# Optimization experiments

Hardware: AMD Instinct MI355X
Metric: run time of the kernel (lower is better)

## Reference

```python
import jax, jax.numpy as jnp
import numpy as np

B_SZ, SEQ = 16, 2048
VOCAB, EMBED = 50257, 128
DSTATE, HID, NCLS = 16, 256, 10
NEDGE = 8192  # edges per graph (avg degree 4)
LN_EPS = 1e-5


def setup_inputs() -> dict:
    key = jax.random.key(0)
    ks = jax.random.split(key, 12)
    tokens = jax.random.randint(ks[0], (B_SZ, SEQ), 0, VOCAB, dtype=jnp.int32)
    lengths = jnp.full((B_SZ,), SEQ, dtype=jnp.int32)  # full-length graphs
    edge_indices = jax.random.randint(ks[1], (B_SZ, 2, NEDGE), 0, SEQ, dtype=jnp.int32)
    emb = (jax.random.normal(ks[2], (VOCAB, EMBED)) * 0.02).at[0].set(0.0)  # padding_idx=0
    A_log = jax.random.normal(ks[3], (EMBED, DSTATE)) * 0.1
    B_w = jax.random.normal(ks[4], (DSTATE, EMBED)) * (1.0 / np.sqrt(EMBED))
    C_w = jax.random.normal(ks[5], (EMBED, DSTATE)) * (1.0 / np.sqrt(DSTATE))
    D_skip = jnp.ones((EMBED,))
    ln_g = jnp.ones((EMBED,))
    ln_b = jnp.zeros((EMBED,))
    Wmsg_w = jax.random.normal(ks[6], (HID, EMBED)) * (1.0 / np.sqrt(EMBED))
    Wupd_w = jax.random.normal(ks[7], (HID, EMBED + HID)) * (1.0 / np.sqrt(EMBED + HID))
    Wupd_b = jax.random.normal(ks[8], (HID,)) * 0.01
    cls_w = jax.random.normal(ks[9], (NCLS, HID)) * (1.0 / np.sqrt(HID))
    cls_b = jnp.zeros((NCLS,))
    return {"tokens": tokens, "lengths": lengths, "edge_indices": edge_indices,
            "emb": emb, "A_log": A_log, "B_w": B_w, "C_w": C_w, "D_skip": D_skip,
            "ln_g": ln_g, "ln_b": ln_b, "Wmsg_w": Wmsg_w, "Wupd_w": Wupd_w,
            "Wupd_b": Wupd_b, "cls_w": cls_w, "cls_b": cls_b}


def _ssm(x, A_log, B_w, C_w, D_skip, ln_g, ln_b):
    # x: (B, S, d_model). Diagonal SSM: h_t = h_{t-1}*exp(A) + B x_t (broadcast over d_model)
    Aexp = jnp.exp(-jnp.exp(A_log))  # (d_model, d_state)
    h0 = jnp.zeros((x.shape[0], EMBED, DSTATE), dtype=x.dtype)

    def step(h, x_t):  # x_t: (B, d_model)
        b_t = x_t @ B_w.T                            # (B, d_state)
        h = h * Aexp[None] + b_t[:, None, :]          # (B, d_model, d_state)
        y = h.mean(axis=1) @ C_w.T + D_skip * x_t     # (B, d_model)
        return h, y

    _, ys = jax.lax.scan(step, h0, jnp.swapaxes(x, 0, 1))
    out = jnp.swapaxes(ys, 0, 1)                      # (B, S, d_model)
    mu = out.mean(-1, keepdims=True)
    var = jnp.mean((out - mu) ** 2, axis=-1, keepdims=True)
    return ln_g * (out - mu) * jax.lax.rsqrt(var + LN_EPS) + ln_b


def reference(tokens, lengths, edge_indices, emb, A_log, B_w, C_w, D_skip,
              ln_g, ln_b, Wmsg_w, Wupd_w, Wupd_b, cls_w, cls_b):
    x = emb[tokens]                                   # (B, S, E)
    h = _ssm(x, A_log, B_w, C_w, D_skip, ln_g, ln_b)  # (B, S, E)
    src, dst = edge_indices[:, 0, :], edge_indices[:, 1, :]   # (B, Ne)
    h_src = jnp.take_along_axis(h, src[:, :, None], axis=1)   # (B, Ne, E)
    msgs = jnp.einsum('bed,hd->beh', h_src, Wmsg_w)            # (B, Ne, H)
    flat_dst = (jnp.arange(B_SZ, dtype=dst.dtype)[:, None] * SEQ + dst).reshape(-1)
    agg = jax.ops.segment_sum(msgs.reshape(-1, HID), flat_dst,
                              num_segments=B_SZ * SEQ).reshape(B_SZ, SEQ, HID)
    upd = jax.nn.relu(jnp.concatenate([h, agg], axis=-1) @ Wupd_w.T + Wupd_b)  # (B, S, H)
    pooled = upd.mean(axis=1)                          # (B, H)  (all lengths == SEQ)
    return pooled @ cls_w.T + cls_b                    # (B, NCLS)
```

## Files before the change

### kernel.cpp

```cpp
#include <hip/hip_runtime.h>

#define B_SZ   16
#define SEQ    2048
#define VOCAB  50257
#define EMBED  128
#define DSTATE 16
#define HID    256
#define NCLS   10
#define NEDGE  8192
#define KTR    64
#define LN_EPS 1e-5f
#define NROW   (B_SZ*SEQ)
#define BCAP   32
#define OVCAP  1024

#define PB_CAST   4096
#define PB_BUCKET (PB_CAST + 512)
#define PB_PRECM  (PB_BUCKET + 128)
#define PB_CTAB   (PB_PRECM + 16)
#define PB_TOTAL  (PB_CTAB + 1)

typedef float  f32x4 __attribute__((ext_vector_type(4)));
typedef short  s16x8 __attribute__((ext_vector_type(8)));

__device__ __forceinline__ float scrub(float x){
  return (x == x && fabsf(x) < 1e30f) ? x : 0.f;
}
__device__ __forceinline__ short f2b(float f){
  unsigned int u = __float_as_uint(f);
  unsigned int r = (u + 0x7fffu + ((u >> 16) & 1u)) >> 16;
  return (short)r;
}
__device__ __forceinline__ unsigned int pack2(float a, float b){
  return (unsigned int)(unsigned short)f2b(a)
       | ((unsigned int)(unsigned short)f2b(b) << 16);
}
__device__ __forceinline__ float lo2f(unsigned int v){ return __uint_as_float(v << 16); }
__device__ __forceinline__ float hi2f(unsigned int v){ return __uint_as_float(v & 0xffff0000u); }

__global__ __launch_bounds__(256) void k_prep(
    const int* __restrict__ tokens, const float* __restrict__ emb,
    const float* __restrict__ A_log, const float* __restrict__ B_w,
    const float* __restrict__ Wmsg, const float* __restrict__ Wupd,
    const int* __restrict__ edges,
    float* __restrict__ c_tab, short* __restrict__ Bf, float* __restrict__ MT,
    unsigned int* __restrict__ x_bf, int* __restrict__ cnt,
    unsigned short* __restrict__ bucket, int* __restrict__ ovf_cnt,
    int* __restrict__ ovf){
  int bid = blockIdx.x, tid = threadIdx.x;
  if (bid < PB_CAST){
    int gid = bid*256 + tid;
    int row = gid >> 5, ch = gid & 31;
    int tok = tokens[row];
    tok = tok < 0 ? 0 : (tok >= VOCAB ? VOCAB-1 : tok);
    float4 v = *(const float4*)(emb + (size_t)tok*EMBED + ch*4);
    uint2 o; o.x = pack2(v.x, v.y); o.y = pack2(v.z, v.w);
    *(uint2*)(x_bf + (size_t)row*(EMBED/2) + ch*2) = o;
  } else if (bid < PB_BUCKET){
    int eid = (bid-PB_CAST)*256 + tid;
    int b = eid >> 13, i = eid & (NEDGE-1);
    const int* ei = edges + (size_t)b*2*NEDGE;
    int s = ei[i]         & (SEQ-1);
    int d = ei[NEDGE + i] & (SEQ-1);
    int gdst = (b << 11) | d;
    int slot = atomicAdd(&cnt[gdst], 1);
    if (slot < BCAP) bucket[(size_t)gdst*BCAP + slot] = (unsigned short)s;
    else {
      int o = atomicAdd(ovf_cnt, 1);
      if (o < OVCAP) ovf[o] = ((b << 11) | s) | (gdst << 16);
    }
  } else if (bid < PB_PRECM){
    int hp = (bid-PB_BUCKET)*2 + (tid >> 7);
    int e  = tid & 127;
    const float* w2 = Wupd + (size_t)hp*384 + 128;
    float acc = 0.f;
    for (int h1 = 0; h1 < HID; ++h1)
      acc += Wmsg[h1*EMBED + e] * w2[h1];
    MT[(size_t)hp*EMBED + e] = scrub(acc);
  } else if (bid < PB_CTAB){
    if (tid < 64){
      int d = bid - PB_PRECM, lane = tid;
      float a0 = scrub(expf(-expf(A_log[(2*lane+0)*DSTATE + d])));
      float a1 = scrub(expf(-expf(A_log[(2*lane+1)*DSTATE + d])));
      float p0 = 1.f, p1 = 1.f;
      for (int k = 0; k < KTR; ++k){
        float s = p0 + p1;
        for (int off = 32; off; off >>= 1) s += __shfl_down(s, off);
        if (lane == 0) c_tab[k*DSTATE + d] = scrub(s * (1.0f/128.0f));
        p0 *= a0; p1 *= a1;
      }
    }
  } else {
    int idx = tid;
    int c = idx >> 6, lane = idx & 63;
    int n = lane & 15;
    int kb = c*32 + (lane >> 4)*8;
    short v[8];
    #pragma unroll
    for (int jj = 0; jj < 8; ++jj) v[jj] = f2b(B_w[(size_t)n*EMBED + kb + jj]);
    *(s16x8*)(Bf + (size_t)idx*8) = *(s16x8*)v;
  }
}

__global__ __launch_bounds__(256) void k_ssm_fused(
    const short* __restrict__ x_bf, const float* __restrict__ c_tab,
    const float* __restrict__ C_w, const float* __restrict__ D_skip,
    const float* __restrict__ ln_g, const float* __restrict__ ln_b,
    const short* __restrict__ Bf, const float* __restrict__ Wupd,
    const float* __restrict__ MT, unsigned int* __restrict__ h_out,
    short* __restrict__ Wcs){
  __shared__ float bsh[128][18];
  __shared__ float msh[64][18];
  __shared__ float Ct[DSTATE][EMBED+2];
  __shared__ float csh[KTR][DSTATE];
  int bid = blockIdx.x, tid = threadIdx.x;

  if (bid >= 512){
    int idx = (bid-512)*256 + tid;
    int c    = idx >> 10;
    int rem  = idx & 1023;
    int j    = rem >> 6;
    int lane = rem & 63;
    int n  = j*16 + (lane & 15);
    int kb = c*32 + (lane >> 4)*8;
    short v[8];
    #pragma unroll
    for (int jj = 0; jj < 8; ++jj){
      int k = kb + jj;
      float val = (k < 128) ? Wupd[(size_t)n*384 + k] : MT[(size_t)n*EMBED + (k-128)];
      v[jj] = f2b(val);
    }
    *(s16x8*)(Wcs + (size_t)idx*8) = *(s16x8*)v;
    return;
  }

  int b  = bid >> 5;
  int t0 = (bid & 31) * 64;
  for (int i = tid; i < DSTATE*EMBED; i += 256){
    int e = i >> 4, d = i & 15;
    Ct[d][e] = C_w[i];
  }
  for (int i = tid; i < KTR*DSTATE; i += 256)
    csh[i >> 4][i & 15] = c_tab[i];

  int wv = tid >> 6, lane = tid & 63;
  int m = lane & 15, lg = lane >> 4;

  const s16x8* Bp = (const s16x8*)Bf;
  #pragma unroll
  for (int tt = 0; tt < 2; ++tt){
    int tile = wv*2 + tt;
    int trow = t0 - 64 + tile*16;
    f32x4 acc = (f32x4){0.f,0.f,0.f,0.f};
    if (trow >= 0){
      const short* xrow = x_bf + ((size_t)(b*SEQ + trow + m))*EMBED + lg*8;
      #pragma unroll
      for (int c = 0; c < 4; ++c){
        s16x8 a = *(const s16x8*)(xrow + c*32);
        acc = __builtin_amdgcn_mfma_f32_16x16x32_bf16(a, Bp[c*64 + lane], acc, 0, 0, 0);
      }
    }
    #pragma unroll
    for (int r = 0; r < 4; ++r)
      bsh[tile*16 + lg*4 + r][m] = scrub(acc[r]);
  }
  __syncthreads();

  {
    int d = tid & 15;
    #pragma unroll
    for (int it = 0; it < 4; ++it){
      int q = (tid + it*256) >> 4;
      int t = t0 + q;
      int base = 64 + q;
      int kmax = (t+1 < KTR) ? t+1 : KTR;
      float acc = 0.f;
      for (int k = 0; k < kmax; ++k) acc += csh[k][d] * bsh[base-k][d];
      msh[q][d] = scrub(acc);
    }
  }
  __syncthreads();

  int e0 = lane*2;
  float2 dsk = *(const float2*)&D_skip[e0];
  float2 lgv = *(const float2*)&ln_g[e0];
  float2 lbv = *(const float2*)&ln_b[e0];
  const unsigned int* xb = (const unsigned int*)x_bf;
  for (int q = wv*16; q < wv*16+16; ++q){
    int row = b*SEQ + t0 + q;
    unsigned int xp = xb[(size_t)row*(EMBED/2) + lane];
    float x0 = lo2f(xp), x1 = hi2f(xp);
    float y0 = dsk.x*x0, y1 = dsk.y*x1;
    #pragma unroll
    for (int d = 0; d < DSTATE; ++d){
      float md = msh[q][d];
      y0 += md * Ct[d][e0];
      y1 += md * Ct[d][e0+1];
    }
    y0 = scrub(y0); y1 = scrub(y1);
    float s = y0+y1, s2 = y0*y0 + y1*y1;
    for (int off = 32; off; off >>= 1){ s += __shfl_down(s,off); s2 += __shfl_down(s2,off); }
    s = __shfl(s, 0); s2 = __shfl(s2, 0);
    float mu  = s * (1.f/EMBED);
    float var = s2 * (1.f/EMBED) - mu*mu;
    float inv = rsqrtf(fmaxf(var, 0.f) + LN_EPS);
    float o0 = scrub(lgv.x*(y0-mu)*inv + lbv.x);
    float o1 = scrub(lgv.y*(y1-mu)*inv + lbv.y);
    h_out[(size_t)row*(EMBED/2) + lane] = pack2(o0, o1);
  }
}

__global__ __launch_bounds__(256) void k_gather(
    const int* __restrict__ cnt, const unsigned short* __restrict__ bucket,
    const int* __restrict__ ovf_cnt, const int* __restrict__ ovf,
    const unsigned int* __restrict__ h, unsigned int* __restrict__ g){
  int wv = threadIdx.x >> 6, lane = threadIdx.x & 63;
  int gdst = blockIdx.x*4 + wv;
  int n = cnt[gdst]; n = n > BCAP ? BCAP : n;
  int b = gdst >> 11;
  const unsigned int* hb = h + (size_t)b*SEQ*(EMBED/2);
  const unsigned short* bk = bucket + (size_t)gdst*BCAP;
  float ax = 0.f, ay = 0.f;
  for (int i = 0; i < n; ++i){
    unsigned int v = hb[(size_t)bk[i]*(EMBED/2) + lane];
    ax += lo2f(v); ay += hi2f(v);
  }
  int on = *ovf_cnt; on = on > OVCAP ? OVCAP : on;
  for (int idx = 0; idx < on; ++idx){
    int pk = ovf[idx];
    if (((pk >> 16) & 0x7fff) == gdst){
      unsigned int v = h[(size_t)(pk & 0xffff)*(EMBED/2) + lane];
      ax += lo2f(v); ay += hi2f(v);
    }
  }
  g[(size_t)gdst*(EMBED/2) + lane] = pack2(scrub(ax), scrub(ay));
}

__global__ __launch_bounds__(256) void k_upd_mfma(
    const short* __restrict__ h, const short* __restrict__ g,
    const short* __restrict__ Wcs, const float* __restrict__ Wupd_b,
    float* __restrict__ pool){
  int tid = threadIdx.x;
  int wave = blockIdx.x*4 + (tid >> 6);
  int lane = tid & 63;
  int row0 = wave * 16;
  int b = row0 >> 11;
  int m = lane & 15, lg = lane >> 4;
  const short* hrow = h + (size_t)(row0+m)*EMBED + lg*8;
  const short* grow = g + (size_t)(row0+m)*EMBED + lg*8;

  f32x4 acc[16];
  #pragma unroll
  for (int j = 0; j < 16; ++j) acc[j] = (f32x4){0.f,0.f,0.f,0.f};

  const s16x8* Bp = (const s16x8*)Wcs;
  #pragma unroll
  for (int c = 0; c < 8; ++c){
    s16x8 a = (c < 4) ? *(const s16x8*)(hrow + c*32)
                      : *(const s16x8*)(grow + (c-4)*32);
    #pragma unroll
    for (int j = 0; j < 16; ++j){
      s16x8 bfr = Bp[(c*16 + j)*64 + lane];
      acc[j] = __builtin_amdgcn_mfma_f32_16x16x32_bf16(a, bfr, acc[j], 0, 0, 0);
    }
  }

  #pragma unroll
  for (int j = 0; j < 16; ++j){
    int n = j*16 + (lane & 15);
    float bias = Wupd_b[n];
    float v = 0.f;
    #pragma unroll
    for (int r = 0; r < 4; ++r) v += fmaxf(acc[j][r] + bias, 0.f);
    v += __shfl_down(v, 32);
    v += __shfl_down(v, 16);
    if (lane < 16) atomicAdd(&pool[b*HID + n], scrub(v));
  }
}

__global__ void k_cls(const float* __restrict__ pool, const float* __restrict__ cls_w,
                      const float* __restrict__ cls_b, float* __restrict__ out){
  int tid = threadIdx.x;
  if (tid >= B_SZ*NCLS) return;
  int b = tid / NCLS, c = tid - b*NCLS;
  const float* p = pool + b*HID;
  const float* w = cls_w + c*HID;
  float s = 0.f;
  for (int h1 = 0; h1 < HID; ++h1) s += p[h1]*w[h1];
  out[tid] = scrub(s * (1.0f/SEQ) + cls_b[c]);
}

extern "C" void kernel_launch(void* const* d_in, const int* in_sizes, int n_in,
                              void* d_out, int out_size, void* d_ws, size_t ws_size,
                              hipStream_t stream) {
  const int*   tokens = (const int*)d_in[0];
  const int*   edges  = (const int*)d_in[2];
  const float* emb    = (const float*)d_in[3];
  const float* A_log  = (const float*)d_in[4];
  const float* B_w    = (const float*)d_in[5];
  const float* C_w    = (const float*)d_in[6];
  const float* D_skip = (const float*)d_in[7];
  const float* ln_g   = (const float*)d_in[8];
  const float* ln_b   = (const float*)d_in[9];
  const float* Wmsg   = (const float*)d_in[10];
  const float* Wupd   = (const float*)d_in[11];
  const float* Wupd_b = (const float*)d_in[12];
  const float* cls_w  = (const float*)d_in[13];
  const float* cls_b  = (const float*)d_in[14];
  float* out = (float*)d_out;

  char* ws = (char*)d_ws;
  float* c_tab = (float*)ws;  ws += 16*1024;
  float* MT    = (float*)ws;  ws += (size_t)HID*EMBED*4;
  short* Wcs   = (short*)ws;  ws += (size_t)HID*HID*2;
  short* Bf    = (short*)ws;  ws += 16*1024;
  char*  zbase = ws;
  float* pool  = (float*)ws;  ws += (size_t)B_SZ*HID*4;
  int*   cnt   = (int*)ws;    ws += (size_t)NROW*4;
  int*   ovf_cnt = (int*)ws;  ws += 64;
  int*   ovf   = (int*)ws;    ws += OVCAP*4;
  size_t zlen = (size_t)((char*)ws - zbase);
  unsigned short* bucket = (unsigned short*)ws; ws += (size_t)NROW*BCAP*2;
  short* x_bf  = (short*)ws;  ws += (size_t)NROW*EMBED*2;
  short* h_bf  = (short*)ws;  ws += (size_t)NROW*EMBED*2;
  short* g_bf  = (short*)ws;  ws += (size_t)NROW*EMBED*2;

  hipMemsetAsync(zbase, 0, zlen, stream);
  hipLaunchKernelGGL(k_prep, dim3(PB_TOTAL), dim3(256), 0, stream,
                     tokens, emb, A_log, B_w, Wmsg, Wupd, edges,
                     c_tab, Bf, MT, (unsigned int*)x_bf, cnt, bucket, ovf_cnt, ovf);
  hipLaunchKernelGGL(k_ssm_fused, dim3(544), dim3(256), 0, stream,
                     x_bf, c_tab, C_w, D_skip, ln_g, ln_b, Bf, Wupd, MT,
                     (unsigned int*)h_bf, Wcs);
  hipLaunchKernelGGL(k_gather, dim3(NROW/4), dim3(256), 0, stream,
                     cnt, bucket, ovf_cnt, ovf, (const unsigned int*)h_bf,
                     (unsigned int*)g_bf);
  hipLaunchKernelGGL(k_upd_mfma, dim3(NROW/64), dim3(256), 0, stream,
                     h_bf, g_bf, Wcs, Wupd_b, pool);
  hipLaunchKernelGGL(k_cls, dim3(1), dim3(256), 0, stream, pool, cls_w, cls_b, out);
}
```

Measured before the change: 193.4 us.

## Fuse gather, update GEMM and classifier into one kernel; register-tile SSM conv

Merges the neighbor-gather, update MFMA and classifier kernels into a single kernel. Each wave gathers neighbor rows directly into MFMA A-fragments in registers instead of writing and rereading a g buffer. Pooled sums are reduced in shared memory before one atomic per block, and a last-block-done counter runs the classifier, which removes two launches. Separately, the SSM causal convolution now computes four outputs per thread with a sliding register window over a fixed-length unrolled loop. The costs are heavier register pressure from the 32-float gather accumulator, and gather loads per lane are less coalesced (16-byte chunks per row rather than a whole wave reading one row).

```diff
diff --git a/kernel.cpp b/kernel.cpp
--- a/kernel.cpp
+++ b/kernel.cpp
@@ -167,17 +167,22 @@
   __syncthreads();
 
   {
-    int d = tid & 15;
-    #pragma unroll
-    for (int it = 0; it < 4; ++it){
-      int q = (tid + it*256) >> 4;
-      int t = t0 + q;
-      int base = 64 + q;
-      int kmax = (t+1 < KTR) ? t+1 : KTR;
-      float acc = 0.f;
-      for (int k = 0; k < kmax; ++k) acc += csh[k][d] * bsh[base-k][d];
-      msh[q][d] = scrub(acc);
-    }
+    int d  = tid & 15;
+    int qb = (tid >> 4) * 4;
+    float a0=0.f, a1=0.f, a2=0.f, a3=0.f;
+    float w0 = bsh[64+qb+0][d];
+    float w1 = bsh[64+qb+1][d];
+    float w2 = bsh[64+qb+2][d];
+    float w3 = bsh[64+qb+3][d];
+    #pragma unroll
+    for (int k = 0; k < KTR; ++k){
+      float c = csh[k][d];
+      a0 += c*w0; a1 += c*w1; a2 += c*w2; a3 += c*w3;
+      w3 = w2; w2 = w1; w1 = w0;
+      w0 = (k+1 < KTR) ? bsh[64+qb-k-1][d] : 0.f;
+    }
+    msh[qb+0][d] = scrub(a0); msh[qb+1][d] = scrub(a1);
+    msh[qb+2][d] = scrub(a2); msh[qb+3][d] = scrub(a3);
   }
   __syncthreads();
 
@@ -210,54 +215,79 @@
   }
 }
 
-__global__ __launch_bounds__(256) void k_gather(
-    const int* __restrict__ cnt, const unsigned short* __restrict__ bucket,
+__global__ __launch_bounds__(256) void k_upd_fused(
+    const short* __restrict__ h, const int* __restrict__ cnt,
+    const unsigned short* __restrict__ bucket,
     const int* __restrict__ ovf_cnt, const int* __restrict__ ovf,
-    const unsigned int* __restrict__ h, unsigned int* __restrict__ g){
-  int wv = threadIdx.x >> 6, lane = threadIdx.x & 63;
-  int gdst = blockIdx.x*4 + wv;
-  int n = cnt[gdst]; n = n > BCAP ? BCAP : n;
-  int b = gdst >> 11;
-  const unsigned int* hb = h + (size_t)b*SEQ*(EMBED/2);
-  const unsigned short* bk = bucket + (size_t)gdst*BCAP;
-  float ax = 0.f, ay = 0.f;
+    const short* __restrict__ Wcs, const float* __restrict__ Wupd_b,
+    float* __restrict__ pool, int* __restrict__ done,
+    const float* __restrict__ cls_w, const float* __restrict__ cls_b,
+    float* __restrict__ out){
+  __shared__ float psum[4][HID];
+  __shared__ float plds[B_SZ*HID];
+  __shared__ int   lastflag;
+  int tid  = threadIdx.x;
+  int wv   = tid >> 6, lane = tid & 63;
+  int wave = blockIdx.x*4 + wv;
+  int row0 = wave * 16;
+  int b    = row0 >> 11;
+  int m = lane & 15, lg = lane >> 4;
+  int r = row0 + m;
+
+  const short* hrow = h + (size_t)r*EMBED + lg*8;
+  s16x8 hfrag[4];
+  #pragma unroll
+  for (int c = 0; c < 4; ++c) hfrag[c] = *(const s16x8*)(hrow + c*32);
+
+  float ge[32];
+  #pragma unroll
+  for (int i = 0; i < 32; ++i) ge[i] = 0.f;
+  int n = cnt[r]; n = n > BCAP ? BCAP : n;
+  const unsigned short* bk = bucket + (size_t)r*BCAP;
+  const short* hb = h + ((size_t)(b << 11))*EMBED;
   for (int i = 0; i < n; ++i){
-    unsigned int v = hb[(size_t)bk[i]*(EMBED/2) + lane];
-    ax += lo2f(v); ay += hi2f(v);
+    int s = bk[i];
+    const short* hs = hb + (size_t)s*EMBED + lg*8;
+    #pragma unroll
+    for (int c = 0; c < 4; ++c){
+      uint4 p = *(const uint4*)(hs + c*32);
+      ge[c*8+0] += lo2f(p.x); ge[c*8+1] += hi2f(p.x);
+      ge[c*8+2] += lo2f(p.y); ge[c*8+3] += hi2f(p.y);
+      ge[c*8+4] += lo2f(p.z); ge[c*8+5] += hi2f(p.z);
+      ge[c*8+6] += lo2f(p.w); ge[c*8+7] += hi2f(p.w);
+    }
   }
   int on = *ovf_cnt; on = on > OVCAP ? OVCAP : on;
   for (int idx = 0; idx < on; ++idx){
     int pk = ovf[idx];
-    if (((pk >> 16) & 0x7fff) == gdst){
-      unsigned int v = h[(size_t)(pk & 0xffff)*(EMBED/2) + lane];
-      ax += lo2f(v); ay += hi2f(v);
-    }
-  }
-  g[(size_t)gdst*(EMBED/2) + lane] = pack2(scrub(ax), scrub(ay));
-}
-
-__global__ __launch_bounds__(256) void k_upd_mfma(
-    const short* __restrict__ h, const short* __restrict__ g,
-    const short* __restrict__ Wcs, const float* __restrict__ Wupd_b,
-    float* __restrict__ pool){
-  int tid = threadIdx.x;
-  int wave = blockIdx.x*4 + (tid >> 6);
-  int lane = tid & 63;
-  int row0 = wave * 16;
-  int b = row0 >> 11;
-  int m = lane & 15, lg = lane >> 4;
-  const short* hrow = h + (size_t)(row0+m)*EMBED + lg*8;
-  const short* grow = g + (size_t)(row0+m)*EMBED + lg*8;
+    if (((pk >> 16) & 0x7fff) == r){
+      const short* hs = h + (size_t)(pk & 0xffff)*EMBED + lg*8;
+      #pragma unroll
+      for (int c = 0; c < 4; ++c){
+        uint4 p = *(const uint4*)(hs + c*32);
+        ge[c*8+0] += lo2f(p.x); ge[c*8+1] += hi2f(p.x);
+        ge[c*8+2] += lo2f(p.y); ge[c*8+3] += hi2f(p.y);
+        ge[c*8+4] += lo2f(p.z); ge[c*8+5] += hi2f(p.z);
+        ge[c*8+6] += lo2f(p.w); ge[c*8+7] += hi2f(p.w);
+      }
+    }
+  }
+  s16x8 gfrag[4];
+  #pragma unroll
+  for (int c = 0; c < 4; ++c){
+    short v[8];
+    #pragma unroll
+    for (int j = 0; j < 8; ++j) v[j] = f2b(scrub(ge[c*8+j]));
+    gfrag[c] = *(s16x8*)v;
+  }
 
   f32x4 acc[16];
   #pragma unroll
   for (int j = 0; j < 16; ++j) acc[j] = (f32x4){0.f,0.f,0.f,0.f};
-
   const s16x8* Bp = (const s16x8*)Wcs;
   #pragma unroll
   for (int c = 0; c < 8; ++c){
-    s16x8 a = (c < 4) ? *(const s16x8*)(hrow + c*32)
-                      : *(const s16x8*)(grow + (c-4)*32);
+    s16x8 a = (c < 4) ? hfrag[c] : gfrag[c-4];
     #pragma unroll
     for (int j = 0; j < 16; ++j){
       s16x8 bfr = Bp[(c*16 + j)*64 + lane];
@@ -267,27 +297,39 @@
 
   #pragma unroll
   for (int j = 0; j < 16; ++j){
-    int n = j*16 + (lane & 15);
-    float bias = Wupd_b[n];
+    int nn = j*16 + m;
+    float bias = Wupd_b[nn];
     float v = 0.f;
     #pragma unroll
-    for (int r = 0; r < 4; ++r) v += fmaxf(acc[j][r] + bias, 0.f);
+    for (int rr = 0; rr < 4; ++rr) v += fmaxf(acc[j][rr] + bias, 0.f);
     v += __shfl_down(v, 32);
     v += __shfl_down(v, 16);
-    if (lane < 16) atomicAdd(&pool[b*HID + n], scrub(v));
-  }
-}
-
-__global__ void k_cls(const float* __restrict__ pool, const float* __restrict__ cls_w,
-                      const float* __restrict__ cls_b, float* __restrict__ out){
-  int tid = threadIdx.x;
-  if (tid >= B_SZ*NCLS) return;
-  int b = tid / NCLS, c = tid - b*NCLS;
-  const float* p = pool + b*HID;
-  const float* w = cls_w + c*HID;
-  float s = 0.f;
-  for (int h1 = 0; h1 < HID; ++h1) s += p[h1]*w[h1];
-  out[tid] = scrub(s * (1.0f/SEQ) + cls_b[c]);
+    if (lane < 16) psum[wv][nn] = scrub(v);
+  }
+  __syncthreads();
+  if (tid < HID){
+    float t = psum[0][tid] + psum[1][tid] + psum[2][tid] + psum[3][tid];
+    atomicAdd(&pool[b*HID + tid], t);
+  }
+  __threadfence();
+  __syncthreads();
+  if (tid == 0){
+    int prev = atomicAdd(done, 1);
+    lastflag = (prev == (int)gridDim.x - 1);
+  }
+  __syncthreads();
+  if (!lastflag) return;
+
+  for (int i = tid; i < B_SZ*HID; i += 256)
+    plds[i] = __hip_atomic_load(&pool[i], __ATOMIC_RELAXED, __HIP_MEMORY_SCOPE_AGENT);
+  __syncthreads();
+  if (tid < B_SZ*NCLS){
+    int bb = tid / NCLS, c = tid - bb*NCLS;
+    const float* w = cls_w + c*HID;
+    float s = 0.f;
+    for (int h1 = 0; h1 < HID; ++h1) s += plds[bb*HID + h1] * w[h1];
+    out[tid] = scrub(s * (1.0f/SEQ) + cls_b[c]);
+  }
 }
 
 extern "C" void kernel_launch(void* const* d_in, const int* in_sizes, int n_in,
@@ -318,12 +360,12 @@
   float* pool  = (float*)ws;  ws += (size_t)B_SZ*HID*4;
   int*   cnt   = (int*)ws;    ws += (size_t)NROW*4;
   int*   ovf_cnt = (int*)ws;  ws += 64;
+  int*   done  = (int*)ws;    ws += 64;
   int*   ovf   = (int*)ws;    ws += OVCAP*4;
   size_t zlen = (size_t)((char*)ws - zbase);
   unsigned short* bucket = (unsigned short*)ws; ws += (size_t)NROW*BCAP*2;
   short* x_bf  = (short*)ws;  ws += (size_t)NROW*EMBED*2;
   short* h_bf  = (short*)ws;  ws += (size_t)NROW*EMBED*2;
-  short* g_bf  = (short*)ws;  ws += (size_t)NROW*EMBED*2;
 
   hipMemsetAsync(zbase, 0, zlen, stream);
   hipLaunchKernelGGL(k_prep, dim3(PB_TOTAL), dim3(256), 0, stream,
@@ -332,10 +374,7 @@
   hipLaunchKernelGGL(k_ssm_fused, dim3(544), dim3(256), 0, stream,
                      x_bf, c_tab, C_w, D_skip, ln_g, ln_b, Bf, Wupd, MT,
                      (unsigned int*)h_bf, Wcs);
-  hipLaunchKernelGGL(k_gather, dim3(NROW/4), dim3(256), 0, stream,
-                     cnt, bucket, ovf_cnt, ovf, (const unsigned int*)h_bf,
-                     (unsigned int*)g_bf);
-  hipLaunchKernelGGL(k_upd_mfma, dim3(NROW/64), dim3(256), 0, stream,
-                     h_bf, g_bf, Wcs, Wupd_b, pool);
-  hipLaunchKernelGGL(k_cls, dim3(1), dim3(256), 0, stream, pool, cls_w, cls_b, out);
-}
+  hipLaunchKernelGGL(k_upd_fused, dim3(NROW/64), dim3(256), 0, stream,
+                     h_bf, cnt, bucket, ovf_cnt, ovf, Wcs, Wupd_b,
+                     pool, done, cls_w, cls_b, out);
+}
```

New measurement: 201.8 us. 4.3% more time.

## Fuse classifier into update kernel via last-block pattern; register-blocked truncated conv

Applied to the files above, without the earlier changes.

Merges the classifier kernel into the update kernel: each block first reduces its four waves' pooled partial sums in shared memory, then issues one atomic per hidden unit, and the last block to finish (tracked by an atomic counter) computes the logits. This removes one kernel launch and cuts global atomics by four. Separately, the truncated SSM convolution now computes four consecutive outputs per thread with a sliding register window over a fully unrolled 64-tap loop, which reuses loaded B values and avoids the variable-trip loop. The risks are higher register pressure and relying on threadfence plus counter ordering for correctness.

```diff
diff --git a/kernel.cpp b/kernel.cpp
--- a/kernel.cpp
+++ b/kernel.cpp
@@ -167,17 +167,22 @@
   __syncthreads();
 
   {
-    int d = tid & 15;
-    #pragma unroll
-    for (int it = 0; it < 4; ++it){
-      int q = (tid + it*256) >> 4;
-      int t = t0 + q;
-      int base = 64 + q;
-      int kmax = (t+1 < KTR) ? t+1 : KTR;
-      float acc = 0.f;
-      for (int k = 0; k < kmax; ++k) acc += csh[k][d] * bsh[base-k][d];
-      msh[q][d] = scrub(acc);
-    }
+    int d  = tid & 15;
+    int qb = (tid >> 4) * 4;
+    float a0=0.f, a1=0.f, a2=0.f, a3=0.f;
+    float w0 = bsh[64+qb+0][d];
+    float w1 = bsh[64+qb+1][d];
+    float w2 = bsh[64+qb+2][d];
+    float w3 = bsh[64+qb+3][d];
+    #pragma unroll
+    for (int k = 0; k < KTR; ++k){
+      float c = csh[k][d];
+      a0 += c*w0; a1 += c*w1; a2 += c*w2; a3 += c*w3;
+      w3 = w2; w2 = w1; w1 = w0;
+      w0 = (k+1 < KTR) ? bsh[64+qb-k-1][d] : 0.f;
+    }
+    msh[qb+0][d] = scrub(a0); msh[qb+1][d] = scrub(a1);
+    msh[qb+2][d] = scrub(a2); msh[qb+3][d] = scrub(a3);
   }
   __syncthreads();
 
@@ -236,13 +241,18 @@
   g[(size_t)gdst*(EMBED/2) + lane] = pack2(scrub(ax), scrub(ay));
 }
 
-__global__ __launch_bounds__(256) void k_upd_mfma(
+__global__ __launch_bounds__(256) void k_upd_fused(
     const short* __restrict__ h, const short* __restrict__ g,
     const short* __restrict__ Wcs, const float* __restrict__ Wupd_b,
-    float* __restrict__ pool){
+    float* __restrict__ pool, int* __restrict__ done,
+    const float* __restrict__ cls_w, const float* __restrict__ cls_b,
+    float* __restrict__ out){
+  __shared__ float psum[4][HID];
+  __shared__ float plds[B_SZ*HID];
+  __shared__ int   lastflag;
   int tid = threadIdx.x;
-  int wave = blockIdx.x*4 + (tid >> 6);
-  int lane = tid & 63;
+  int wv = tid >> 6, lane = tid & 63;
+  int wave = blockIdx.x*4 + wv;
   int row0 = wave * 16;
   int b = row0 >> 11;
   int m = lane & 15, lg = lane >> 4;
@@ -267,27 +277,39 @@
 
   #pragma unroll
   for (int j = 0; j < 16; ++j){
-    int n = j*16 + (lane & 15);
+    int n = j*16 + m;
     float bias = Wupd_b[n];
     float v = 0.f;
     #pragma unroll
     for (int r = 0; r < 4; ++r) v += fmaxf(acc[j][r] + bias, 0.f);
     v += __shfl_down(v, 32);
     v += __shfl_down(v, 16);
-    if (lane < 16) atomicAdd(&pool[b*HID + n], scrub(v));
-  }
-}
-
-__global__ void k_cls(const float* __restrict__ pool, const float* __restrict__ cls_w,
-                      const float* __restrict__ cls_b, float* __restrict__ out){
-  int tid = threadIdx.x;
-  if (tid >= B_SZ*NCLS) return;
-  int b = tid / NCLS, c = tid - b*NCLS;
-  const float* p = pool + b*HID;
-  const float* w = cls_w + c*HID;
-  float s = 0.f;
-  for (int h1 = 0; h1 < HID; ++h1) s += p[h1]*w[h1];
-  out[tid] = scrub(s * (1.0f/SEQ) + cls_b[c]);
+    if (lane < 16) psum[wv][n] = scrub(v);
+  }
+  __syncthreads();
+  if (tid < HID){
+    float t = psum[0][tid] + psum[1][tid] + psum[2][tid] + psum[3][tid];
+    atomicAdd(&pool[b*HID + tid], t);
+  }
+  __threadfence();
+  __syncthreads();
+  if (tid == 0){
+    int prev = atomicAdd(done, 1);
+    lastflag = (prev == (int)gridDim.x - 1);
+  }
+  __syncthreads();
+  if (!lastflag) return;
+
+  for (int i = tid; i < B_SZ*HID; i += 256)
+    plds[i] = __hip_atomic_load(&pool[i], __ATOMIC_RELAXED, __HIP_MEMORY_SCOPE_AGENT);
+  __syncthreads();
+  if (tid < B_SZ*NCLS){
+    int bb = tid / NCLS, c = tid - bb*NCLS;
+    const float* w = cls_w + c*HID;
+    float s = 0.f;
+    for (int h1 = 0; h1 < HID; ++h1) s += plds[bb*HID + h1] * w[h1];
+    out[tid] = scrub(s * (1.0f/SEQ) + cls_b[c]);
+  }
 }
 
 extern "C" void kernel_launch(void* const* d_in, const int* in_sizes, int n_in,
@@ -318,6 +340,7 @@
   float* pool  = (float*)ws;  ws += (size_t)B_SZ*HID*4;
   int*   cnt   = (int*)ws;    ws += (size_t)NROW*4;
   int*   ovf_cnt = (int*)ws;  ws += 64;
+  int*   done  = (int*)ws;    ws += 64;
   int*   ovf   = (int*)ws;    ws += OVCAP*4;
   size_t zlen = (size_t)((char*)ws - zbase);
   unsigned short* bucket = (unsigned short*)ws; ws += (size_t)NROW*BCAP*2;
@@ -335,7 +358,6 @@
   hipLaunchKernelGGL(k_gather, dim3(NROW/4), dim3(256), 0, stream,
                      cnt, bucket, ovf_cnt, ovf, (const unsigned int*)h_bf,
                      (unsigned int*)g_bf);
-  hipLaunchKernelGGL(k_upd_mfma, dim3(NROW/64), dim3(256), 0, stream,
-                     h_bf, g_bf, Wcs, Wupd_b, pool);
-  hipLaunchKernelGGL(k_cls, dim3(1), dim3(256), 0, stream, pool, cls_w, cls_b, out);
-}
+  hipLaunchKernelGGL(k_upd_fused, dim3(NROW/64), dim3(256), 0, stream,
+                     h_bf, g_bf, Wcs, Wupd_b, pool, done, cls_w, cls_b, out);
+}
```

After: 220.4 us. 13.9% more time.
